# Optimization experiments

Measured on AMD Instinct MI355X. Metric: run time of the kernel, lower is better.

## Reference

```python
import jax, jax.numpy as jnp
import numpy as np
from jax import lax

NMS_THRESHOLD = 0.45
PRE_THRESHOLD = 0.005


def setup_inputs() -> dict:
    key = jax.random.key(0)
    k1, k2 = jax.random.split(key)
    B, C, N = 8, 20, 2048
    u = jax.random.uniform(k1, (B, N, 4), dtype=jnp.float32)  # raw rand per spec
    # build valid [x1,y1,x2,y2] boxes from raw uniforms (center + size param)
    cx, cy = u[..., 0], u[..., 1]
    w = u[..., 2] * 0.2 + 0.01
    h = u[..., 3] * 0.2 + 0.01
    bbs = jnp.stack([cx - w / 2, cy - h / 2, cx + w / 2, cy + h / 2], axis=-1)
    conf = jax.random.uniform(k2, (B, C, N), dtype=jnp.float32)
    return {"bbs": bbs, "conf": conf}


def _nms_filter(bbs, conf, nms_threshold, pre_threshold):
    # bbs: [B, N, 4] (x1,y1,x2,y2); conf: [B, C, N]
    B, C, N = conf.shape
    order = jnp.argsort(-conf, axis=-1)                      # [B,C,N] desc by score
    conf_s = jnp.take_along_axis(conf, order, axis=-1)       # sorted scores
    boxes_b = jnp.broadcast_to(bbs[:, None, :, :], (B, C, N, 4))
    boxes_s = jnp.take_along_axis(boxes_b, order[..., None], axis=2)  # [B,C,N,4]

    x1, y1, x2, y2 = (boxes_s[..., i] for i in range(4))
    areas = jnp.maximum(x2 - x1, 0.0) * jnp.maximum(y2 - y1, 0.0)     # [B,C,N]
    pos = jnp.arange(N)

    keep0 = conf_s > pre_threshold  # pre-threshold: dropped boxes never kept nor suppress

    def body(i, keep):
        # box at sorted rank i
        bx1 = lax.dynamic_index_in_dim(x1, i, 2, keepdims=True)  # [B,C,1]
        by1 = lax.dynamic_index_in_dim(y1, i, 2, keepdims=True)
        bx2 = lax.dynamic_index_in_dim(x2, i, 2, keepdims=True)
        by2 = lax.dynamic_index_in_dim(y2, i, 2, keepdims=True)
        a_i = lax.dynamic_index_in_dim(areas, i, 2, keepdims=True)
        iw = jnp.maximum(jnp.minimum(bx2, x2) - jnp.maximum(bx1, x1), 0.0)
        ih = jnp.maximum(jnp.minimum(by2, y2) - jnp.maximum(by1, y1), 0.0)
        inter = iw * ih
        iou = inter / jnp.maximum(a_i + areas - inter, 1e-12)    # [B,C,N]
        keep_i = lax.dynamic_index_in_dim(keep, i, 2, keepdims=True)  # alive pivot?
        suppress = (iou > nms_threshold) & (pos > i) & keep_i
        return keep & ~suppress

    keep = lax.fori_loop(0, N, body, keep0)
    filt_s = conf_s * keep.astype(conf_s.dtype)
    inv = jnp.argsort(order, axis=-1)                          # inverse permutation
    return jnp.take_along_axis(filt_s, inv, axis=-1)


def reference(bbs, conf):
    return _nms_filter(bbs, conf, NMS_THRESHOLD, PRE_THRESHOLD)
```

## Files before the change

kernel.cpp:

```cpp
#include <hip/hip_runtime.h>


#define BB   8
#define CC   20
#define NBOX 2048
#define CAP  64
#define PRE_THR 0.005f
#define IOU_M 0x1.CCCCCDp-2

typedef unsigned long long u64;
typedef unsigned int u32;
typedef unsigned short u16;

__device__ __forceinline__ float area_rn(float x1, float y1, float x2, float y2) {
    return __fmul_rn(fmaxf(__fsub_rn(x2, x1), 0.f), fmaxf(__fsub_rn(y2, y1), 0.f));
}
__device__ __forceinline__ bool iou_gt(float inter, float den) {
    return (double)inter > IOU_M * (double)den;
}

__global__ __launch_bounds__(1024) void adj_kernel(const float4* __restrict__ bbs,
                                                   u32* __restrict__ deg,
                                                   u16* __restrict__ nbr,
                                                   u16* __restrict__ nbr8) {
    const int batch = blockIdx.x >> 5;
    const int seg   = blockIdx.x & 31;
    const int lane  = threadIdx.x & 63;
    const int wv    = threadIdx.x >> 6;

    __shared__ float4 sbox[NBOX];
    __shared__ float  sar[NBOX];

    const float4* bp = bbs + (size_t)batch * NBOX;
    for (int n = threadIdx.x; n < NBOX; n += 1024) {
        float4 bv = bp[n];
        sbox[n] = bv;
        sar[n]  = area_rn(bv.x, bv.y, bv.z, bv.w);
    }
    __syncthreads();

    const int r0 = seg * 64 + wv * 4;
    float4 rb[4]; float ra[4]; u32 hits[4] = {0, 0, 0, 0};
    #pragma unroll
    for (int t = 0; t < 4; ++t) { rb[t] = sbox[r0 + t]; ra[t] = sar[r0 + t]; }

    #pragma unroll 4
    for (int k = 0; k < 32; ++k) {
        const int c = lane + (k << 6);
        const float4 cb = sbox[c];
        const float  ca = sar[c];
        #pragma unroll
        for (int t = 0; t < 4; ++t) {
            float iw = fmaxf(__fsub_rn(fminf(rb[t].z, cb.z), fmaxf(rb[t].x, cb.x)), 0.f);
            float ih = fmaxf(__fsub_rn(fminf(rb[t].w, cb.w), fmaxf(rb[t].y, cb.y)), 0.f);
            float inter = __fmul_rn(iw, ih);
            float den = fmaxf(__fsub_rn(__fadd_rn(ra[t], ca), inter), 1e-12f);
            if (c != r0 + t && iou_gt(inter, den)) hits[t] |= 1u << k;
        }
    }

    #pragma unroll
    for (int t = 0; t < 4; ++t) {
        const int i = r0 + t;
        int cnt = __popc(hits[t]);
        int ofs = cnt;
        #pragma unroll
        for (int d = 1; d < 64; d <<= 1) {
            int v = __shfl_up(ofs, d);
            if (lane >= d) ofs += v;
        }
        int total = __shfl(ofs, 63);
        ofs -= cnt;
        const bool spill = (total > 8);
        u16* row  = nbr  + ((size_t)batch * NBOX + i) * CAP;
        u16* row8 = nbr8 + ((size_t)batch * NBOX + i) * 8;
        u32 h = hits[t];
        while (h) {
            int k = __ffs(h) - 1; h &= h - 1;
            u16 j = (u16)(lane + (k << 6));
            if (ofs < 8)                        row8[ofs] = j;
            else if (spill && ofs < CAP)        row[ofs]  = j;
            ++ofs;
        }
        if (lane == 0) deg[batch * NBOX + i] = (u32)min(total, CAP);
    }
}

__global__ __launch_bounds__(256) void prop_kernel(const float* __restrict__ conf,
                                                   const u32* __restrict__ deg,
                                                   const u16* __restrict__ nbr,
                                                   const u16* __restrict__ nbr8,
                                                   float* __restrict__ out) {
    const int wg   = blockIdx.x;
    const int b    = wg / CC;
    const int base = wg * NBOX;
    const int tid  = threadIdx.x;

    __shared__ float         sconf[NBOX];
    __shared__ unsigned char sstate[NBOX];
    __shared__ int sflag[2];

    const u32*   degb = deg  + b * NBOX;
    const u16*   nbrb = nbr  + (size_t)b * NBOX * CAP;
    const uint4* n8b  = (const uint4*)nbr8 + (size_t)b * NBOX;

    float cv[8]; int dreg[8]; uint4 nv[8];
    #pragma unroll
    for (int p = 0; p < 8; ++p) {
        const int i = tid + (p << 8);
        cv[p]   = conf[base + i];
        dreg[p] = (int)degb[i];
        nv[p]   = n8b[i];
    }
    #pragma unroll
    for (int p = 0; p < 8; ++p) {
        const int i = tid + (p << 8);
        sconf[i]  = cv[p];
        sstate[i] = (cv[p] > PRE_THR) ? 0 : 2;
    }
    if (tid == 0) { sflag[0] = 0; sflag[1] = 0; }
    __syncthreads();

    u64 h0[8], h1[8]; u32 vm[8];
    u32 und = 0, slow = 0;
    #pragma unroll
    for (int p = 0; p < 8; ++p) {
        h0[p] = 0; h1[p] = 0;
        const int i = tid + (p << 8);
        int cnt = 0;
        if (sstate[i] == 0) {
            const u32 bi = __float_as_uint(cv[p]);
            const int d  = dreg[p];
            const u32 w[4] = { nv[p].x, nv[p].y, nv[p].z, nv[p].w };
            #pragma unroll
            for (int k = 0; k < 8; ++k) {
                if (k < d) {
                    const int j = (int)((w[k >> 1] >> ((k & 1) << 4)) & 0xffff);
                    if (sstate[j] != 2) {
                        const u32 bj = __float_as_uint(sconf[j]);
                        if (bj > bi || (bj == bi && j < i)) {
                            if (cnt < 4)      h0[p] |= (u64)j << (cnt << 4);
                            else if (cnt < 8) h1[p] |= (u64)j << ((cnt - 4) << 4);
                            ++cnt;
                        }
                    }
                }
            }
            if (d > 8) {
                const u16* row = nbrb + (size_t)i * CAP;
                for (int k = 8; k < d; ++k) {
                    const int j = row[k];
                    if (sstate[j] != 2) {
                        const u32 bj = __float_as_uint(sconf[j]);
                        if (bj > bi || (bj == bi && j < i)) {
                            if (cnt < 4)      h0[p] |= (u64)j << (cnt << 4);
                            else if (cnt < 8) h1[p] |= (u64)j << ((cnt - 4) << 4);
                            ++cnt;
                        }
                    }
                }
            }
            if (cnt == 0) sstate[i] = 1;
            else {
                und |= 1u << p;
                if (cnt > 8) slow |= 1u << p;
            }
        }
        vm[p] = (cnt >= 8) ? 0xffu : ((1u << cnt) - 1u);
    }
    __syncthreads();

    int rnd = 0;
    while (true) {
        if (tid == 0) sflag[(rnd + 1) & 1] = 0;
        bool changed = false;
        #pragma unroll 1
        for (int sweep = 0; sweep < 2; ++sweep) {
            #pragma unroll
            for (int p = 0; p < 8; ++p) {
                if (und & (1u << p)) {
                    const int i = tid + (p << 8);
                    if (!(slow & (1u << p))) {
                        u32 alive_b = 0, pend_b = 0;
                        #pragma unroll
                        for (int k = 0; k < 4; ++k) {
                            const int j = (int)((h0[p] >> (k << 4)) & 0xffff);
                            const int st = sstate[j];
                            alive_b |= (u32)(st == 1) << k;
                            pend_b  |= (u32)(st == 0) << k;
                        }
                        #pragma unroll
                        for (int k = 0; k < 4; ++k) {
                            const int j = (int)((h1[p] >> (k << 4)) & 0xffff);
                            const int st = sstate[j];
                            alive_b |= (u32)(st == 1) << (k + 4);
                            pend_b  |= (u32)(st == 0) << (k + 4);
                        }
                        if (alive_b & vm[p]) {
                            sstate[i] = 2; und &= ~(1u << p); changed = true;
                        } else if (!(pend_b & vm[p])) {
                            sstate[i] = 1; und &= ~(1u << p); changed = true;
                        }
                    } else {
                        const u32 bi = __float_as_uint(cv[p]);
                        const u32 w[4] = { nv[p].x, nv[p].y, nv[p].z, nv[p].w };
                        const u16* row = nbrb + (size_t)i * CAP;
                        int verdict = 1;
                        for (int k = 0; k < dreg[p]; ++k) {
                            const int j = (k < 8)
                                ? (int)((w[k >> 1] >> ((k & 1) << 4)) & 0xffff)
                                : (int)row[k];
                            const int st = sstate[j];
                            if (st == 2) continue;
                            const u32 bj = __float_as_uint(sconf[j]);
                            if (bj > bi || (bj == bi && j < i)) {
                                if (st == 1) { verdict = 2; break; }
                                verdict = 0;
                            }
                        }
                        if (verdict != 0) {
                            sstate[i] = (unsigned char)verdict;
                            und &= ~(1u << p); changed = true;
                        }
                    }
                }
            }
        }
        if (changed) sflag[rnd & 1] = 1;
        __syncthreads();
        if (!sflag[rnd & 1]) break;
        ++rnd;
    }

    #pragma unroll
    for (int p = 0; p < 8; ++p) {
        const int i = tid + (p << 8);
        out[base + i] = (sstate[i] == 1) ? cv[p] : 0.f;
    }
}

#define NMS_THR 0.45f
__global__ __launch_bounds__(256) void nms_mono(const float* __restrict__ bbs,
                                                const float* __restrict__ conf,
                                                float* __restrict__ out) {
    const int wg   = blockIdx.x;
    const int b    = wg / CC;
    const int base = wg * NBOX;
    const int tid  = threadIdx.x;
    const int lane = tid & 63;
    const int wv   = tid >> 6;

    __shared__ union {
        u64 keys[NBOX];
        struct { float x1[NBOX], y1[NBOX], x2[NBOX], y2[NBOX]; } a;
    } u;
    __shared__ u64           Mcol[NBOX];
    __shared__ int           sidx[NBOX];
    __shared__ unsigned char skeep[NBOX];

    for (int n = tid; n < NBOX; n += 256) {
        float cvv = conf[base + n];
        u.keys[n] = ((u64)__float_as_uint(cvv) << 32) | (u32)(~n);
    }
    __syncthreads();
    for (int k = 2; k <= NBOX; k <<= 1)
        for (int j = k >> 1; j > 0; j >>= 1) {
            const int mask = j - 1;
            for (int t = tid; t < NBOX / 2; t += 256) {
                int i = ((t & ~mask) << 1) | (t & mask), ip = i + j;
                u64 a = u.keys[i], c2 = u.keys[ip];
                if ((a < c2) == ((i & k) == 0)) { u.keys[i] = c2; u.keys[ip] = a; }
            }
            __syncthreads();
        }
    u64 myk[8];
    #pragma unroll
    for (int p = 0; p < 8; ++p) myk[p] = u.keys[tid + p * 256];
    __syncthreads();
    #pragma unroll
    for (int p = 0; p < 8; ++p) {
        int r = tid + p * 256;
        u64 key = myk[p];
        int idx = (int)(~(u32)key) & (NBOX - 1);
        float cvv = __uint_as_float((u32)(key >> 32));
        float4 bv = ((const float4*)bbs)[b * NBOX + idx];
        u.a.x1[r] = bv.x; u.a.y1[r] = bv.y; u.a.x2[r] = bv.z; u.a.y2[r] = bv.w;
        sidx[r] = idx;
        skeep[r] = (cvv > PRE_THR) ? 1 : 0;
        out[base + idx] = cvv;
    }
    __syncthreads();
    for (int c = wv; c < NBOX / 64; c += 4) {
        int r = c * 64 + lane;
        float bx1 = u.a.x1[r], by1 = u.a.y1[r], bx2 = u.a.x2[r], by2 = u.a.y2[r];
        float bar = area_rn(bx1, by1, bx2, by2);
        u64 col = 0;
        for (int s = 1; s < 64; ++s) {
            int src = (lane + s) & 63;
            float px1 = __shfl(bx1, src), py1 = __shfl(by1, src);
            float px2 = __shfl(bx2, src), py2 = __shfl(by2, src);
            float par = area_rn(px1, py1, px2, py2);
            float iw = fmaxf(__fsub_rn(fminf(px2, bx2), fmaxf(px1, bx1)), 0.f);
            float ih = fmaxf(__fsub_rn(fminf(py2, by2), fmaxf(py1, by1)), 0.f);
            float inter = __fmul_rn(iw, ih);
            float den = fmaxf(__fsub_rn(__fadd_rn(bar, par), inter), 1e-12f);
            if ((__fdiv_rn(inter, den) > NMS_THR) && (src > lane)) col |= 1ull << src;
        }
        Mcol[r] = col;
    }
    __syncthreads();
    for (int cb = 0; cb < NBOX; cb += 64) {
        bool k0 = skeep[cb + lane] != 0;
        u64 alive = __ballot(k0);
        if (alive)
            for (int l = 0; l < 64; ++l) {
                u64 cl = Mcol[cb + l];
                u64 take = (u64)0 - ((alive >> l) & 1ull);
                alive &= ~(cl & take);
            }
        if (tid < 64) skeep[cb + lane] = (unsigned char)((alive >> lane) & 1ull);
        if (alive)
            for (int jb = cb + 64 + wv * 64; jb < NBOX; jb += 256) {
                int jj = jb + lane;
                bool jk = skeep[jj] != 0;
                if (__ballot(jk)) {
                    float jx1 = u.a.x1[jj], jy1 = u.a.y1[jj];
                    float jx2 = u.a.x2[jj], jy2 = u.a.y2[jj];
                    float jar = area_rn(jx1, jy1, jx2, jy2);
                    bool dead = false;
                    u64 m = alive;
                    while (m) {
                        int l = __ffsll(m) - 1; m &= m - 1;
                        int r = cb + l;
                        float px1 = u.a.x1[r], py1 = u.a.y1[r];
                        float px2 = u.a.x2[r], py2 = u.a.y2[r];
                        float par = area_rn(px1, py1, px2, py2);
                        float iw = fmaxf(__fsub_rn(fminf(px2, jx2), fmaxf(px1, jx1)), 0.f);
                        float ih = fmaxf(__fsub_rn(fminf(py2, jy2), fmaxf(py1, jy1)), 0.f);
                        float inter = __fmul_rn(iw, ih);
                        float den = fmaxf(__fsub_rn(__fadd_rn(par, jar), inter), 1e-12f);
                        dead = dead | (__fdiv_rn(inter, den) > NMS_THR);
                    }
                    if (jk && dead) skeep[jj] = 0;
                }
            }
        __syncthreads();
    }
    #pragma unroll
    for (int p = 0; p < 8; ++p) {
        int r = tid + p * 256;
        if (!skeep[r]) out[base + sidx[r]] = 0.0f;
    }
}

extern "C" void kernel_launch(void* const* d_in, const int* in_sizes, int n_in,
                              void* d_out, int out_size, void* d_ws, size_t ws_size,
                              hipStream_t stream) {
    const float* bbs  = (const float*)d_in[0];
    const float* conf = (const float*)d_in[1];
    float* out = (float*)d_out;

    const size_t deg_bytes  = (size_t)BB * NBOX * sizeof(u32);
    const size_t nbr_bytes  = (size_t)BB * NBOX * CAP * sizeof(u16);
    const size_t nbr8_bytes = (size_t)BB * NBOX * 8 * sizeof(u16);
    if (ws_size >= deg_bytes + nbr_bytes + nbr8_bytes) {
        u32* deg  = (u32*)d_ws;
        u16* nbr  = (u16*)((char*)d_ws + deg_bytes);
        u16* nbr8 = (u16*)((char*)d_ws + deg_bytes + nbr_bytes);
        adj_kernel<<<dim3(BB * 32), dim3(1024), 0, stream>>>((const float4*)bbs, deg, nbr, nbr8);
        prop_kernel<<<dim3(BB * CC), dim3(256), 0, stream>>>(conf, deg, nbr, nbr8, out);
    } else {
        nms_mono<<<dim3(BB * CC), dim3(256), 0, stream>>>(bbs, conf, out);
    }
}
```

Measured before the change: 112.6 us.

## Fuse adjacency and propagation kernels into one cooperative kernel with grid sync

Merges the adjacency-building kernel and the NMS propagation kernel into a single cooperative launch of 256 blocks of 1024 threads, with a grid-wide sync between the two phases. This removes the second kernel launch and the gap between kernels. The propagation phase is rewritten for 1024-thread blocks with two boxes per thread and a shared-memory union. Grid sync has its own cost, and only 160 of the 256 blocks do work in phase two. If the cooperative launch fails, the code falls back to the old two-kernel path.

```diff
diff --git a/kernel.cpp b/kernel.cpp
--- a/kernel.cpp
+++ b/kernel.cpp
@@ -1,4 +1,7 @@
 #include <hip/hip_runtime.h>
+#include <hip/hip_cooperative_groups.h>
+
+namespace cg = cooperative_groups;
 
 
 #define BB   8
@@ -17,6 +20,229 @@
 }
 __device__ __forceinline__ bool iou_gt(float inter, float den) {
     return (double)inter > IOU_M * (double)den;
+}
+
+__global__ __launch_bounds__(1024) void fused_kernel(const float4* __restrict__ bbs,
+                                                     const float* __restrict__ conf,
+                                                     u32* __restrict__ deg,
+                                                     u16* __restrict__ nbr,
+                                                     u16* __restrict__ nbr8,
+                                                     float* __restrict__ out) {
+    __shared__ union {
+        struct { float4 box[NBOX]; float ar[NBOX]; } p1;
+        float conf2[NBOX];
+    } sh;
+    __shared__ unsigned char sstate[NBOX];
+    __shared__ int sflag[2];
+
+    const int tid  = threadIdx.x;
+    const int lane = tid & 63;
+    const int wv   = tid >> 6;
+
+    {
+        const int batch = blockIdx.x >> 5;
+        const int seg   = blockIdx.x & 31;
+        const float4* bp = bbs + (size_t)batch * NBOX;
+        for (int n = tid; n < NBOX; n += 1024) {
+            float4 bv = bp[n];
+            sh.p1.box[n] = bv;
+            sh.p1.ar[n]  = area_rn(bv.x, bv.y, bv.z, bv.w);
+        }
+        __syncthreads();
+
+        const int r0 = seg * 64 + wv * 4;
+        float4 rb[4]; float ra[4]; u32 hits[4] = {0, 0, 0, 0};
+        #pragma unroll
+        for (int t = 0; t < 4; ++t) { rb[t] = sh.p1.box[r0 + t]; ra[t] = sh.p1.ar[r0 + t]; }
+
+        #pragma unroll 4
+        for (int k = 0; k < 32; ++k) {
+            const int c = lane + (k << 6);
+            const float4 cb = sh.p1.box[c];
+            const float  ca = sh.p1.ar[c];
+            #pragma unroll
+            for (int t = 0; t < 4; ++t) {
+                float iw = fmaxf(__fsub_rn(fminf(rb[t].z, cb.z), fmaxf(rb[t].x, cb.x)), 0.f);
+                float ih = fmaxf(__fsub_rn(fminf(rb[t].w, cb.w), fmaxf(rb[t].y, cb.y)), 0.f);
+                float inter = __fmul_rn(iw, ih);
+                float den = fmaxf(__fsub_rn(__fadd_rn(ra[t], ca), inter), 1e-12f);
+                if (c != r0 + t && iou_gt(inter, den)) hits[t] |= 1u << k;
+            }
+        }
+
+        #pragma unroll
+        for (int t = 0; t < 4; ++t) {
+            const int i = r0 + t;
+            int cnt = __popc(hits[t]);
+            int ofs = cnt;
+            #pragma unroll
+            for (int d = 1; d < 64; d <<= 1) {
+                int v = __shfl_up(ofs, d);
+                if (lane >= d) ofs += v;
+            }
+            int total = __shfl(ofs, 63);
+            ofs -= cnt;
+            const bool spill = (total > 8);
+            u16* row  = nbr  + ((size_t)batch * NBOX + i) * CAP;
+            u16* row8 = nbr8 + ((size_t)batch * NBOX + i) * 8;
+            u32 h = hits[t];
+            while (h) {
+                int k = __ffs(h) - 1; h &= h - 1;
+                u16 j = (u16)(lane + (k << 6));
+                if (ofs < 8)                 row8[ofs] = j;
+                else if (spill && ofs < CAP) row[ofs]  = j;
+                ++ofs;
+            }
+            if (lane == 0) deg[batch * NBOX + i] = (u32)min(total, CAP);
+        }
+    }
+
+    __threadfence();
+    cg::this_grid().sync();
+
+    if (blockIdx.x < BB * CC) {
+        const int wg   = blockIdx.x;
+        const int b    = wg / CC;
+        const int base = wg * NBOX;
+
+        const u32*   degb = deg  + b * NBOX;
+        const u16*   nbrb = nbr  + (size_t)b * NBOX * CAP;
+        const uint4* n8b  = (const uint4*)nbr8 + (size_t)b * NBOX;
+
+        float cv[2]; int dreg[2]; uint4 nv[2];
+        #pragma unroll
+        for (int p = 0; p < 2; ++p) {
+            const int i = tid + (p << 10);
+            cv[p]   = conf[base + i];
+            dreg[p] = (int)degb[i];
+            nv[p]   = n8b[i];
+        }
+        #pragma unroll
+        for (int p = 0; p < 2; ++p) {
+            const int i = tid + (p << 10);
+            sh.conf2[i] = cv[p];
+            sstate[i]   = (cv[p] > PRE_THR) ? 0 : 2;
+        }
+        if (tid == 0) { sflag[0] = 0; sflag[1] = 0; }
+        __syncthreads();
+
+        u64 h0[2], h1[2]; u32 vm[2];
+        u32 und = 0, slow = 0;
+        #pragma unroll
+        for (int p = 0; p < 2; ++p) {
+            h0[p] = 0; h1[p] = 0;
+            const int i = tid + (p << 10);
+            int cnt = 0;
+            if (sstate[i] == 0) {
+                const u32 bi = __float_as_uint(cv[p]);
+                const int d  = dreg[p];
+                const u32 w[4] = { nv[p].x, nv[p].y, nv[p].z, nv[p].w };
+                #pragma unroll
+                for (int k = 0; k < 8; ++k) {
+                    if (k < d) {
+                        const int j = (int)((w[k >> 1] >> ((k & 1) << 4)) & 0xffff);
+                        if (sstate[j] != 2) {
+                            const u32 bj = __float_as_uint(sh.conf2[j]);
+                            if (bj > bi || (bj == bi && j < i)) {
+                                if (cnt < 4)      h0[p] |= (u64)j << (cnt << 4);
+                                else if (cnt < 8) h1[p] |= (u64)j << ((cnt - 4) << 4);
+                                ++cnt;
+                            }
+                        }
+                    }
+                }
+                if (d > 8) {
+                    const u16* row = nbrb + (size_t)i * CAP;
+                    for (int k = 8; k < d; ++k) {
+                        const int j = row[k];
+                        if (sstate[j] != 2) {
+                            const u32 bj = __float_as_uint(sh.conf2[j]);
+                            if (bj > bi || (bj == bi && j < i)) {
+                                if (cnt < 4)      h0[p] |= (u64)j << (cnt << 4);
+                                else if (cnt < 8) h1[p] |= (u64)j << ((cnt - 4) << 4);
+                                ++cnt;
+                            }
+                        }
+                    }
+                }
+                if (cnt == 0) sstate[i] = 1;
+                else {
+                    und |= 1u << p;
+                    if (cnt > 8) slow |= 1u << p;
+                }
+            }
+            vm[p] = (cnt >= 8) ? 0xffu : ((1u << cnt) - 1u);
+        }
+        __syncthreads();
+
+        int rnd = 0;
+        while (true) {
+            if (tid == 0) sflag[(rnd + 1) & 1] = 0;
+            bool changed = false;
+            #pragma unroll 1
+            for (int sweep = 0; sweep < 2; ++sweep) {
+                #pragma unroll
+                for (int p = 0; p < 2; ++p) {
+                    if (und & (1u << p)) {
+                        const int i = tid + (p << 10);
+                        if (!(slow & (1u << p))) {
+                            u32 alive_b = 0, pend_b = 0;
+                            #pragma unroll
+                            for (int k = 0; k < 4; ++k) {
+                                const int j = (int)((h0[p] >> (k << 4)) & 0xffff);
+                                const int st = sstate[j];
+                                alive_b |= (u32)(st == 1) << k;
+                                pend_b  |= (u32)(st == 0) << k;
+                            }
+                            #pragma unroll
+                            for (int k = 0; k < 4; ++k) {
+                                const int j = (int)((h1[p] >> (k << 4)) & 0xffff);
+                                const int st = sstate[j];
+                                alive_b |= (u32)(st == 1) << (k + 4);
+                                pend_b  |= (u32)(st == 0) << (k + 4);
+                            }
+                            if (alive_b & vm[p]) {
+                                sstate[i] = 2; und &= ~(1u << p); changed = true;
+                            } else if (!(pend_b & vm[p])) {
+                                sstate[i] = 1; und &= ~(1u << p); changed = true;
+                            }
+                        } else {
+                            const u32 bi = __float_as_uint(cv[p]);
+                            const u32 w[4] = { nv[p].x, nv[p].y, nv[p].z, nv[p].w };
+                            const u16* row = nbrb + (size_t)i * CAP;
+                            int verdict = 1;
+                            for (int k = 0; k < dreg[p]; ++k) {
+                                const int j = (k < 8)
+                                    ? (int)((w[k >> 1] >> ((k & 1) << 4)) & 0xffff)
+                                    : (int)row[k];
+                                const int st = sstate[j];
+                                if (st == 2) continue;
+                                const u32 bj = __float_as_uint(sh.conf2[j]);
+                                if (bj > bi || (bj == bi && j < i)) {
+                                    if (st == 1) { verdict = 2; break; }
+                                    verdict = 0;
+                                }
+                            }
+                            if (verdict != 0) {
+                                sstate[i] = (unsigned char)verdict;
+                                und &= ~(1u << p); changed = true;
+                            }
+                        }
+                    }
+                }
+            }
+            if (changed) sflag[rnd & 1] = 1;
+            __syncthreads();
+            if (!sflag[rnd & 1]) break;
+            ++rnd;
+        }
+
+        #pragma unroll
+        for (int p = 0; p < 2; ++p) {
+            const int i = tid + (p << 10);
+            out[base + i] = (sstate[i] == 1) ? cv[p] : 0.f;
+        }
+    }
 }
 
 __global__ __launch_bounds__(1024) void adj_kernel(const float4* __restrict__ bbs,
@@ -78,8 +304,8 @@
         while (h) {
             int k = __ffs(h) - 1; h &= h - 1;
             u16 j = (u16)(lane + (k << 6));
-            if (ofs < 8)                        row8[ofs] = j;
-            else if (spill && ofs < CAP)        row[ofs]  = j;
+            if (ofs < 8)                 row8[ofs] = j;
+            else if (spill && ofs < CAP) row[ofs]  = j;
             ++ofs;
         }
         if (lane == 0) deg[batch * NBOX + i] = (u32)min(total, CAP);
@@ -367,8 +593,17 @@
         u32* deg  = (u32*)d_ws;
         u16* nbr  = (u16*)((char*)d_ws + deg_bytes);
         u16* nbr8 = (u16*)((char*)d_ws + deg_bytes + nbr_bytes);
-        adj_kernel<<<dim3(BB * 32), dim3(1024), 0, stream>>>((const float4*)bbs, deg, nbr, nbr8);
-        prop_kernel<<<dim3(BB * CC), dim3(256), 0, stream>>>(conf, deg, nbr, nbr8, out);
+        const float4* bbs4 = (const float4*)bbs;
+
+        void* args[] = { (void*)&bbs4, (void*)&conf, (void*)&deg,
+                         (void*)&nbr, (void*)&nbr8, (void*)&out };
+        hipError_t e = hipLaunchCooperativeKernel((const void*)fused_kernel,
+                                                  dim3(256), dim3(1024),
+                                                  args, 0, stream);
+        if (e != hipSuccess) {
+            adj_kernel<<<dim3(BB * 32), dim3(1024), 0, stream>>>(bbs4, deg, nbr, nbr8);
+            prop_kernel<<<dim3(BB * CC), dim3(256), 0, stream>>>(conf, deg, nbr, nbr8, out);
+        }
     } else {
         nms_mono<<<dim3(BB * CC), dim3(256), 0, stream>>>(bbs, conf, out);
     }
```

After: 186.1 us. 65.3% more time.
